# Performance work log

Measured on AMD Instinct MI355X. Metric: run time of the kernel, lower is better.

## Reference

```python
import jax, jax.numpy as jnp
import numpy as np

B, S, D = 1, 4096, 896
NH, NKV, HD = 14, 2, 64
ROPE_BASE = 1000000.0

def rotate_half(x):
    x1, x2 = x[..., :x.shape[-1] // 2], x[..., x.shape[-1] // 2:]
    return jnp.concatenate((-x2, x1), axis=-1)

def rope_tables(seq_len, head_dim, base):
    inv_freq = 1.0 / (base ** (jnp.arange(0, head_dim, 2, dtype=jnp.float32) / head_dim))
    t = jnp.arange(seq_len, dtype=jnp.float32)
    freqs = jnp.einsum('i,j->ij', t, inv_freq)
    emb = jnp.concatenate((freqs, freqs), axis=-1)  # [S, HD]
    return jnp.cos(emb), jnp.sin(emb)

def setup_inputs() -> dict:
    key = jax.random.key(0)
    ks = jax.random.split(key, 6)
    hidden_states = jax.random.normal(ks[0], (B, S, D), dtype=jnp.float32)
    # additive causal mask [1,1,S,S]
    neg = jnp.finfo(jnp.float32).min
    causal = jnp.where(jnp.tril(jnp.ones((S, S), dtype=bool)), 0.0, neg)
    attention_mask = causal[None, None, :, :].astype(jnp.float32)
    sc = 0.02
    Wq = jax.random.normal(ks[1], (D, NH * HD), dtype=jnp.float32) * sc
    Wk = jax.random.normal(ks[2], (D, NKV * HD), dtype=jnp.float32) * sc
    Wv = jax.random.normal(ks[3], (D, NKV * HD), dtype=jnp.float32) * sc
    Wo = jax.random.normal(ks[4], (D, D), dtype=jnp.float32) * sc
    bq = jnp.zeros((NH * HD,), jnp.float32)
    bk = jnp.zeros((NKV * HD,), jnp.float32)
    bv = jnp.zeros((NKV * HD,), jnp.float32)
    return {"hidden_states": hidden_states, "attention_mask": attention_mask,
            "Wq": Wq, "bq": bq, "Wk": Wk, "bk": bk, "Wv": Wv, "bv": bv, "Wo": Wo}

def reference(hidden_states, attention_mask, Wq, bq, Wk, bk, Wv, bv, Wo):
    b, s, _ = hidden_states.shape
    groups = NH // NKV
    q = (hidden_states @ Wq + bq).reshape(b, s, NH, HD)
    k = (hidden_states @ Wk + bk).reshape(b, s, NKV, HD)
    v = (hidden_states @ Wv + bv).reshape(b, s, NKV, HD)
    cos, sin = rope_tables(s, HD, ROPE_BASE)
    cos = cos[None, :, None, :]
    sin = sin[None, :, None, :]
    q = q * cos + rotate_half(q) * sin
    k = k * cos + rotate_half(k) * sin
    # GQA: repeat KV heads
    k = jnp.repeat(k, groups, axis=2)
    v = jnp.repeat(v, groups, axis=2)
    # [b, h, s, d]
    q = jnp.transpose(q, (0, 2, 1, 3))
    k = jnp.transpose(k, (0, 2, 1, 3))
    v = jnp.transpose(v, (0, 2, 1, 3))
    attn = jnp.einsum('bhqd,bhkd->bhqk', q, k) / jnp.sqrt(jnp.float32(HD))
    attn = attn + attention_mask
    attn = jax.nn.softmax(attn, axis=-1)
    out = jnp.einsum('bhqk,bhkd->bhqd', attn, v)
    out = jnp.transpose(out, (0, 2, 1, 3)).reshape(b, s, NH * HD)
    return out @ Wo
```

## Files before the change

### kernel.cpp

```cpp
#include <hip/hip_runtime.h>
#include <math.h>

constexpr int S_    = 4096;
constexpr int Dm    = 896;
constexpr int NHd   = 14;
constexpr int NKVh  = 2;
constexpr int HDim  = 64;
constexpr int NQ    = NHd * HDim;
constexpr int NK    = NKVh * HDim;
constexpr int NQK   = NQ + NK;
constexpr int GROUPS = NHd / NKVh;
constexpr float L2B   = 19.9315685693241740873f;
constexpr float LOG2E = 1.44269504088896340736f;

constexpr int NUNITS = 952;

typedef __attribute__((ext_vector_type(8)))  short bf16x8;
typedef __attribute__((ext_vector_type(4)))  short bf16x4;
typedef __attribute__((ext_vector_type(4)))  float f32x4;
typedef __attribute__((ext_vector_type(16))) float f32x16;
typedef __attribute__((ext_vector_type(4)))  int   i32x4;

__device__ __forceinline__ short f2bf(float f) {
  unsigned u = __builtin_bit_cast(unsigned, f);
  unsigned r = (u + 0x7FFFu + ((u >> 16) & 1u)) >> 16;
  return (short)r;
}
__device__ __forceinline__ float bf2f(short s) {
  return __builtin_bit_cast(float, ((unsigned)(unsigned short)s) << 16);
}

__device__ __forceinline__ unsigned cvtpk(float lo, float hi) {
  unsigned r;
  asm("v_cvt_pk_bf16_f32 %0, %1, %2" : "=v"(r) : "v"(lo), "v"(hi));
  return r;
}

__device__ __forceinline__ void gload16(const void* g, void* l) {
  __builtin_amdgcn_global_load_lds(
      (const __attribute__((address_space(1))) unsigned int*)g,
      (__attribute__((address_space(3))) unsigned int*)l, 16, 0, 0);
}

__global__ __launch_bounds__(256) void prep_all(
    const float* __restrict__ hs, short* __restrict__ hsb,
    float* __restrict__ cost, float* __restrict__ sint,
    const float* __restrict__ Wq, const float* __restrict__ Wk,
    const float* __restrict__ Wv, const float* __restrict__ Wo,
    short* __restrict__ wtq, short* __restrict__ wto,
    unsigned* __restrict__ cnt)
{
  const int bid = blockIdx.x;
  const int tid = threadIdx.x;
  if (bid == 2751 && tid == 0) *cnt = 0u;
  if (bid < 1792) {
    int idx = bid * 256 + tid;
    float4 a = ((const float4*)hs)[idx * 2];
    float4 b = ((const float4*)hs)[idx * 2 + 1];
    bf16x8 o;
    o[0] = f2bf(a.x); o[1] = f2bf(a.y); o[2] = f2bf(a.z); o[3] = f2bf(a.w);
    o[4] = f2bf(b.x); o[5] = f2bf(b.y); o[6] = f2bf(b.z); o[7] = f2bf(b.w);
    ((bf16x8*)hsb)[idx] = o;
    return;
  }
  if (bid < 2304) {
    int idx = (bid - 1792) * 256 + tid;
    int m = idx >> 5, j = idx & 31;
    float invf = exp2f(-(float)j * (L2B / 32.0f));
    float th = (float)m * invf;
    float s, c;
    sincosf(th, &s, &c);
    cost[idx] = c;
    sint[idx] = s;
    return;
  }
  __shared__ float t[64 * 68];
  const int b2 = bid - 2304;
  const int kt = b2 % 14;
  const int by = b2 / 14;

  const float* src; int srcN, nt; short* dst; int rowOff;
  if (by < 14)      { src = Wq; srcN = NQ; nt = by;      dst = wtq; rowOff = 0; }
  else if (by < 16) { src = Wk; srcN = NK; nt = by - 14; dst = wtq; rowOff = 896; }
  else if (by < 18) { src = Wv; srcN = NK; nt = by - 16; dst = wtq; rowOff = 1024; }
  else              { src = Wo; srcN = NQ; nt = by - 18; dst = wto; rowOff = 0; }

  #pragma unroll
  for (int i = 0; i < 4; i++) {
    int idx = tid + i * 256;
    int r = idx >> 4, c4 = (idx & 15) * 4;
    *(float4*)&t[r * 68 + c4] =
        *(const float4*)&src[(size_t)(kt * 64 + r) * srcN + nt * 64 + c4];
  }
  __syncthreads();
  const int nl = tid >> 2;
  const int kc = (tid & 3) * 16;
  bf16x8 o0, o1;
  #pragma unroll
  for (int i = 0; i < 8; i++) o0[i] = f2bf(t[(kc + i) * 68 + nl]);
  #pragma unroll
  for (int i = 0; i < 8; i++) o1[i] = f2bf(t[(kc + 8 + i) * 68 + nl]);
  short* dp = dst + (size_t)(rowOff + nt * 64 + nl) * 896 + kt * 64 + kc;
  *(bf16x8*)dp = o0;
  *(bf16x8*)(dp + 8) = o1;
}

template<int EPI>
__global__ __launch_bounds__(256) void gemm64(
    const short* __restrict__ A, const short* __restrict__ Bt,
    const float* __restrict__ biasq, const float* __restrict__ biask,
    const float* __restrict__ biasv,
    const float* __restrict__ cost, const float* __restrict__ sint,
    short* __restrict__ qkb, short* __restrict__ vtb,
    float* __restrict__ outp)
{
  __shared__ short Als[64 * 64];
  __shared__ short Bls[128 * 64];
  const int tid = threadIdx.x;
  const int lane = tid & 63;
  const int w = tid >> 6;
  const int wm = w >> 1, wn = w & 1;
  const int r16 = lane & 15, rg = lane >> 4;
  const int bm = blockIdx.x, bn = blockIdx.y;

  const f32x4 zero4 = {0.f, 0.f, 0.f, 0.f};
  f32x4 acc[2][4];
  #pragma unroll
  for (int mt = 0; mt < 2; mt++)
    #pragma unroll
    for (int nt = 0; nt < 4; nt++) acc[mt][nt] = zero4;

  const int srow = (lane >> 3);
  const int scol = (lane & 7) * 8;

  for (int kt = 0; kt < 14; ++kt) {
    __syncthreads();
    #pragma unroll
    for (int i = 0; i < 2; i++) {
      int c = w * 2 + i;
      int row = c * 8 + srow;
      gload16(A + (size_t)(bm * 64 + row) * 896 + kt * 64 + scol, &Als[c * 512]);
    }
    #pragma unroll
    for (int i = 0; i < 4; i++) {
      int c = w * 4 + i;
      int row = c * 8 + srow;
      gload16(Bt + (size_t)(bn * 128 + row) * 896 + kt * 64 + scol, &Bls[c * 512]);
    }
    __syncthreads();

    bf16x8 af[2][2], bfr[4][2];
    #pragma unroll
    for (int mt = 0; mt < 2; mt++)
      #pragma unroll
      for (int ks = 0; ks < 2; ks++)
        af[mt][ks] = *(const bf16x8*)&Als[(wm * 32 + mt * 16 + r16) * 64 + ks * 32 + rg * 8];
    #pragma unroll
    for (int nt = 0; nt < 4; nt++)
      #pragma unroll
      for (int ks = 0; ks < 2; ks++)
        bfr[nt][ks] = *(const bf16x8*)&Bls[(wn * 64 + nt * 16 + r16) * 64 + ks * 32 + rg * 8];
    #pragma unroll
    for (int mt = 0; mt < 2; mt++)
      #pragma unroll
      for (int nt = 0; nt < 4; nt++)
        #pragma unroll
        for (int ks = 0; ks < 2; ks++)
          acc[mt][nt] = __builtin_amdgcn_mfma_f32_16x16x32_bf16(
              af[mt][ks], bfr[nt][ks], acc[mt][nt], 0, 0, 0);
  }

  if (EPI == 0) {
    const int nbase = bn * 128 + wn * 64;
    if (bn < 8) {
      const float scl = (bn < 7) ? (0.125f * LOG2E) : 1.0f;
      const float* bias = (bn < 7) ? biasq : (biask - 896);
      #pragma unroll
      for (int mt = 0; mt < 2; mt++) {
        const int m0 = bm * 64 + wm * 32 + mt * 16 + rg * 4;
        #pragma unroll
        for (int nt = 0; nt < 4; nt++) {
          int n = nbase + nt * 16 + r16;
          int j = n & 31;
          float sgn = (n & 32) ? 1.f : -1.f;
          float b0 = bias[n], b1 = bias[n ^ 32];
          #pragma unroll
          for (int r = 0; r < 4; r++) {
            int m = m0 + r;
            float c_ = cost[m * 32 + j], s_ = sint[m * 32 + j];
            float val = ((acc[mt][nt][r] + b0) * c_ +
                         sgn * (acc[mt][nt ^ 2][r] + b1) * s_) * scl;
            qkb[(size_t)m * NQK + n] = f2bf(val);
          }
        }
      }
    } else {
      #pragma unroll
      for (int mt = 0; mt < 2; mt++) {
        const int m0 = bm * 64 + wm * 32 + mt * 16 + rg * 4;
        #pragma unroll
        for (int nt = 0; nt < 4; nt++) {
          int vc = wn * 64 + nt * 16 + r16;
          float b0 = biasv[vc];
          bf16x4 pk;
          #pragma unroll
          for (int r = 0; r < 4; r++) pk[r] = f2bf(acc[mt][nt][r] + b0);
          *(bf16x4*)&vtb[(size_t)vc * S_ + m0] = pk;
        }
      }
    }
  } else {
    #pragma unroll
    for (int mt = 0; mt < 2; mt++) {
      const int m0 = bm * 64 + wm * 32 + mt * 16 + rg * 4;
      #pragma unroll
      for (int nt = 0; nt < 4; nt++) {
        int n = bn * 128 + wn * 64 + nt * 16 + r16;
        #pragma unroll
        for (int r = 0; r < 4; r++)
          outp[(size_t)(m0 + r) * NQ + n] = acc[mt][nt][r];
      }
    }
  }
}

__global__ __launch_bounds__(256, 3) void flash_mfma(
    const short* __restrict__ qkb, const short* __restrict__ vtb,
    short* __restrict__ attnb, short* __restrict__ orec,
    float* __restrict__ mlrec, unsigned* __restrict__ cnt)
{
  __shared__ __align__(16) char lds[32768];
  __shared__ int s_unit;

  const int tid  = threadIdx.x;
  const int lane = tid & 63;
  const int w    = tid >> 6;
  const int q32  = lane & 31;
  const int hi   = lane >> 5;

  const int c8   = tid & 7;
  const int key0 = tid >> 3;
  const int key1 = key0 + 32;
  const int swz0 = (c8 ^ (key0 & 7)) << 4;
  const int swz1 = (c8 ^ (key1 & 7)) << 4;

  bf16x8 ones;
  #pragma unroll
  for (int j = 0; j < 8; j++) ones[j] = (short)0x3F80;

  for (;;) {
    __syncthreads();
    if (tid == 0) s_unit = (int)atomicAdd(cnt, 1u);
    __syncthreads();
    const int u = s_unit;
    if (u >= NUNITS) break;

    const int e = u / 14;
    const int h = u - e * 14;
    int qt, ci;
    if (e < 36)      { qt = 31 - e / 3; ci = e - (31 - qt) * 3; }
    else if (e < 60) { int f = e - 36; qt = 19 - (f >> 1); ci = f & 1; }
    else             { qt = 67 - e; ci = 0; }
    const int K  = 2 * (qt + 1);
    const int n  = (qt < 8) ? 1 : (qt < 20) ? 2 : 3;
    const int L  = (K + n - 1) / n;
    const int kt_lo = ci * L;
    const int kt_hi = (kt_lo + L < K) ? (kt_lo + L) : K;
    const int kv = h / GROUPS;
    const int q0 = qt * 128;
    const int kbase2 = (NQ + kv * HDim) * 2;
    const int qg = q0 + w * 32 + q32;

    bf16x8 qf[4];
    {
      const short* qp = qkb + (size_t)qg * NQK + h * HDim + hi * 8;
      #pragma unroll
      for (int ks = 0; ks < 4; ++ks) qf[ks] = *(const bf16x8*)(qp + ks * 16);
    }

    f32x16 acc_o[2], acc_l;
    float m_run = 0.f;
    #pragma unroll
    for (int r = 0; r < 16; ++r) { acc_o[0][r] = 0.f; acc_o[1][r] = 0.f; acc_l[r] = 0.f; }

    const char* ksrc0 = (const char*)qkb + (size_t)(kt_lo * 64 + key0) * 2048 + kbase2 + swz0;
    const char* ksrc1 = (const char*)qkb + (size_t)(kt_lo * 64 + key1) * 2048 + kbase2 + swz1;
    const char* vsrc0 = (const char*)vtb + (size_t)(kv * 64 + key0) * 8192 + (size_t)kt_lo * 128 + swz0;
    const char* vsrc1 = (const char*)vtb + (size_t)(kv * 64 + key1) * 8192 + (size_t)kt_lo * 128 + swz1;

    gload16(ksrc0, lds + w * 1024);
    gload16(ksrc1, lds + 4096 + w * 1024);
    gload16(vsrc0, lds + 8192 + w * 1024);
    gload16(vsrc1, lds + 12288 + w * 1024);
    ksrc0 += 131072; ksrc1 += 131072;
    vsrc0 += 128;    vsrc1 += 128;

    for (int kt = kt_lo; kt < kt_hi; ++kt) {
      const int cur = (kt - kt_lo) & 1;
      asm volatile("s_waitcnt vmcnt(0)" ::: "memory");
      __builtin_amdgcn_s_barrier();
      if (kt + 1 < kt_hi) {
        char* B = lds + ((cur ^ 1) << 14);
        gload16(ksrc0, B + w * 1024);
        gload16(ksrc1, B + 4096 + w * 1024);
        gload16(vsrc0, B + 8192 + w * 1024);
        gload16(vsrc1, B + 12288 + w * 1024);
        ksrc0 += 131072; ksrc1 += 131072;
        vsrc0 += 128;    vsrc1 += 128;
      }
      __builtin_amdgcn_sched_barrier(0);
      const char* KsB = lds + (cur << 14);
      const char* VtB = KsB + 8192;
      const int kb = kt * 64;

      f32x16 sc[2];
      #pragma unroll
      for (int r = 0; r < 16; ++r) { sc[0][r] = 0.f; sc[1][r] = 0.f; }
      #pragma unroll
      for (int t = 0; t < 2; ++t) {
        const int key = t * 32 + q32;
        #pragma unroll
        for (int ks = 0; ks < 4; ++ks) {
          bf16x8 kf = *(const bf16x8*)(KsB + key * 128 + (((2 * ks + hi) ^ (key & 7)) << 4));
          sc[t] = __builtin_amdgcn_mfma_f32_32x32x16_bf16(kf, qf[ks], sc[t], 0, 0, 0);
        }
      }

      if (kb + 63 > q0 + w * 32) {
        #pragma unroll
        for (int t = 0; t < 2; ++t)
          #pragma unroll
          for (int r = 0; r < 16; ++r) {
            int key = kb + t * 32 + (r & 3) + 8 * (r >> 2) + 4 * hi;
            sc[t][r] = (key > qg) ? -1e30f : sc[t][r];
          }
      }

      f32x16 mm;
      #pragma unroll
      for (int r = 0; r < 16; ++r) mm[r] = fmaxf(sc[0][r], sc[1][r]);
      #pragma unroll
      for (int r = 0; r < 8; ++r) mm[r] = fmaxf(mm[r], mm[r + 8]);
      #pragma unroll
      for (int r = 0; r < 4; ++r) mm[r] = fmaxf(mm[r], mm[r + 4]);
      float pm = fmaxf(fmaxf(mm[0], mm[1]), fmaxf(mm[2], mm[3]));
      {
        float a = pm, b = pm;
        asm("v_permlane32_swap_b32 %0, %1" : "+v"(a), "+v"(b));
        pm = fmaxf(a, b);
      }

      if (!__all(pm <= m_run + 8.0f)) {
        float newm = fmaxf(m_run, pm);
        float scl = exp2f(m_run - newm);
        m_run = newm;
        acc_l[0] *= scl;
        #pragma unroll
        for (int r = 0; r < 16; ++r) { acc_o[0][r] *= scl; acc_o[1][r] *= scl; }
      }

      #pragma unroll
      for (int t = 0; t < 2; ++t)
        #pragma unroll
        for (int r = 0; r < 16; ++r) sc[t][r] = exp2f(sc[t][r] - m_run);

      unsigned U0[2][4], U1[2][4];
      #pragma unroll
      for (int t = 0; t < 2; ++t)
        #pragma unroll
        for (int a = 0; a < 4; ++a) {
          U0[t][a] = cvtpk(sc[t][4 * a],     sc[t][4 * a + 1]);
          U1[t][a] = cvtpk(sc[t][4 * a + 2], sc[t][4 * a + 3]);
        }

      #pragma unroll
      for (int kp = 0; kp < 4; ++kp) {
        const int t = kp >> 1, c = kp & 1;
        unsigned x0 = U0[t][2 * c], y0 = U0[t][2 * c + 1];
        unsigned x1 = U1[t][2 * c], y1 = U1[t][2 * c + 1];
        asm("v_permlane32_swap_b32 %0, %1" : "+v"(x0), "+v"(y0));
        asm("v_permlane32_swap_b32 %0, %1" : "+v"(x1), "+v"(y1));
        i32x4 pi = {(int)x0, (int)x1, (int)y0, (int)y1};
        bf16x8 pf = __builtin_bit_cast(bf16x8, pi);
        acc_l = __builtin_amdgcn_mfma_f32_32x32x16_bf16(ones, pf, acc_l, 0, 0, 0);
        #pragma unroll
        for (int dt = 0; dt < 2; ++dt) {
          const int d = dt * 32 + q32;
          bf16x8 vf = *(const bf16x8*)(VtB + d * 128 + (((2 * kp + hi) ^ (d & 7)) << 4));
          acc_o[dt] = __builtin_amdgcn_mfma_f32_32x32x16_bf16(vf, pf, acc_o[dt], 0, 0, 0);
        }
      }
    }

    if (n == 1) {
      const float inv = 1.0f / acc_l[0];
      short* op = attnb + (size_t)qg * NQ + h * HDim + 4 * hi;
      #pragma unroll
      for (int dt = 0; dt < 2; ++dt)
        #pragma unroll
        for (int rq = 0; rq < 4; ++rq) {
          bf16x4 pk;
          pk[0] = f2bf(acc_o[dt][4 * rq]     * inv);
          pk[1] = f2bf(acc_o[dt][4 * rq + 1] * inv);
          pk[2] = f2bf(acc_o[dt][4 * rq + 2] * inv);
          pk[3] = f2bf(acc_o[dt][4 * rq + 3] * inv);
          *(bf16x4*)(op + dt * 32 + 8 * rq) = pk;
        }
    } else {
      const int qloc = w * 32 + q32;
      short* op;
      if (ci == 0) {
        op = attnb + (size_t)qg * NQ + h * HDim + 4 * hi;
      } else {
        int er = (qt < 20) ? (h * 36 + (qt - 8))
                           : (h * 36 + 12 + (qt - 20) * 2 + (ci - 1));
        op = orec + (size_t)er * 8192 + (size_t)qloc * 64 + 4 * hi;
      }
      #pragma unroll
      for (int dt = 0; dt < 2; ++dt)
        #pragma unroll
        for (int rq = 0; rq < 4; ++rq) {
          bf16x4 pk;
          pk[0] = f2bf(acc_o[dt][4 * rq]);
          pk[1] = f2bf(acc_o[dt][4 * rq + 1]);
          pk[2] = f2bf(acc_o[dt][4 * rq + 2]);
          pk[3] = f2bf(acc_o[dt][4 * rq + 3]);
          *(bf16x4*)(op + dt * 32 + 8 * rq) = pk;
        }
      if (hi == 0) {
        int co = (qt < 20) ? (8 + (qt - 8) * 2 + ci) : (32 + (qt - 20) * 3 + ci);
        float2 ml = {m_run, acc_l[0]};
        *(float2*)(mlrec + ((size_t)(h * 68 + co) * 128 + qloc) * 2) = ml;
      }
    }
  }
}

__global__ __launch_bounds__(128) void merge_chunks(
    const short* __restrict__ orec, const float* __restrict__ mlrec,
    short* __restrict__ attnb)
{
  const int b = blockIdx.x;
  const int h = b / 24;
  const int qt = 8 + (b - h * 24);
  const int n = (qt < 20) ? 2 : 3;
  const int qloc = threadIdx.x;
  const int q = qt * 128 + qloc;

  const int co0 = (qt < 20) ? (8 + (qt - 8) * 2) : (32 + (qt - 20) * 3);
  float2 ml0 = *(const float2*)(mlrec + ((size_t)(h * 68 + co0)     * 128 + qloc) * 2);
  float2 ml1 = *(const float2*)(mlrec + ((size_t)(h * 68 + co0 + 1) * 128 + qloc) * 2);
  float2 ml2 = (n == 3)
      ? *(const float2*)(mlrec + ((size_t)(h * 68 + co0 + 2) * 128 + qloc) * 2)
      : float2{-3.0e38f, 0.f};

  float M = fmaxf(fmaxf(ml0.x, ml1.x), ml2.x);
  float a0 = exp2f(ml0.x - M), a1 = exp2f(ml1.x - M);
  float a2 = (n == 3) ? exp2f(ml2.x - M) : 0.f;
  float inv = 1.0f / (a0 * ml0.y + a1 * ml1.y + a2 * ml2.y);
  float s0 = a0 * inv, s1 = a1 * inv, s2 = a2 * inv;

  const int er1 = (qt < 20) ? (h * 36 + (qt - 8)) : (h * 36 + 12 + (qt - 20) * 2);
  short* O0 = attnb + (size_t)q * NQ + h * HDim;
  const short* O1 = orec + (size_t)er1 * 8192 + (size_t)qloc * 64;
  const short* O2 = (n == 3) ? (O1 + 8192) : O1;

  #pragma unroll
  for (int i = 0; i < 8; i++) {
    bf16x8 x0 = *(const bf16x8*)(O0 + i * 8);
    bf16x8 x1 = *(const bf16x8*)(O1 + i * 8);
    bf16x8 x2 = *(const bf16x8*)(O2 + i * 8);
    bf16x8 o;
    #pragma unroll
    for (int j = 0; j < 8; j++)
      o[j] = f2bf(s0 * bf2f(x0[j]) + s1 * bf2f(x1[j]) + s2 * bf2f(x2[j]));
    *(bf16x8*)(O0 + i * 8) = o;
  }
}

extern "C" void kernel_launch(void* const* d_in, const int* in_sizes, int n_in,
                              void* d_out, int out_size, void* d_ws, size_t ws_size,
                              hipStream_t stream)
{
  const float* hs = (const float*)d_in[0];
  const float* Wq = (const float*)d_in[2];
  const float* bq = (const float*)d_in[3];
  const float* Wk = (const float*)d_in[4];
  const float* bk = (const float*)d_in[5];
  const float* Wv = (const float*)d_in[6];
  const float* bv = (const float*)d_in[7];
  const float* Wo = (const float*)d_in[8];

  short* hsb  = (short*)d_ws;
  short* wtq  = hsb + (size_t)S_ * Dm;
  short* wto  = wtq + (size_t)1152 * 896;
  float* cost = (float*)(wto + (size_t)896 * 896);
  float* sint = cost + (size_t)S_ * 32;
  short* qkb  = (short*)(sint + (size_t)S_ * 32);
  short* vtb  = qkb + (size_t)S_ * NQK;
  short* attnb= vtb + (size_t)NK * S_;
  float* out  = (float*)d_out;

  short*    orec  = hsb;
  float*    mlrec = cost;
  unsigned* cnt   = (unsigned*)((char*)attnb + (size_t)S_ * NQ * 2);

  hipLaunchKernelGGL(prep_all, dim3(2752), dim3(256), 0, stream,
                     hs, hsb, cost, sint, Wq, Wk, Wv, Wo, wtq, wto, cnt);
  hipLaunchKernelGGL((gemm64<0>), dim3(64, 9), dim3(256), 0, stream,
                     hsb, wtq, bq, bk, bv, cost, sint, qkb, vtb, (float*)nullptr);
  hipLaunchKernelGGL(flash_mfma, dim3(768), dim3(256), 0, stream,
                     qkb, vtb, attnb, orec, mlrec, cnt);
  hipLaunchKernelGGL(merge_chunks, dim3(336), dim3(128), 0, stream,
                     orec, mlrec, attnb);
  hipLaunchKernelGGL((gemm64<1>), dim3(64, 7), dim3(256), 0, stream,
                     attnb, wto, bq, bk, bv, cost, sint,
                     (short*)nullptr, (short*)nullptr, out);
}
```

Baseline: 130.0 us.

## Stage two KV tiles per barrier in flash attention and lower occupancy

The flash attention loop now loads and computes K/V tiles in pairs. A double buffer of two 64-key tiles per stage in a 64KB LDS array halves the number of vmcnt waits and block barriers. To make room for the larger LDS footprint, launch bounds drop from 3 to 2 blocks per SM and the persistent grid shrinks from 768 to 512 blocks. This trades latency hiding from occupancy for fewer synchronisation points and deeper prefetch; each barrier now waits on a larger batch of loads.

After: 131.6 us. No clear change (+1.2%).

```diff
diff --git a/kernel.cpp b/kernel.cpp
--- a/kernel.cpp
+++ b/kernel.cpp
@@ -224,12 +224,12 @@
   }
 }
 
-__global__ __launch_bounds__(256, 3) void flash_mfma(
+__global__ __launch_bounds__(256, 2) void flash_mfma(
     const short* __restrict__ qkb, const short* __restrict__ vtb,
     short* __restrict__ attnb, short* __restrict__ orec,
     float* __restrict__ mlrec, unsigned* __restrict__ cnt)
 {
-  __shared__ __align__(16) char lds[32768];
+  __shared__ __align__(16) char lds[65536];
   __shared__ int s_unit;
 
   const int tid  = threadIdx.x;
@@ -288,31 +288,16 @@
     const char* vsrc0 = (const char*)vtb + (size_t)(kv * 64 + key0) * 8192 + (size_t)kt_lo * 128 + swz0;
     const char* vsrc1 = (const char*)vtb + (size_t)(kv * 64 + key1) * 8192 + (size_t)kt_lo * 128 + swz1;
 
-    gload16(ksrc0, lds + w * 1024);
-    gload16(ksrc1, lds + 4096 + w * 1024);
-    gload16(vsrc0, lds + 8192 + w * 1024);
-    gload16(vsrc1, lds + 12288 + w * 1024);
-    ksrc0 += 131072; ksrc1 += 131072;
-    vsrc0 += 128;    vsrc1 += 128;
-
-    for (int kt = kt_lo; kt < kt_hi; ++kt) {
-      const int cur = (kt - kt_lo) & 1;
-      asm volatile("s_waitcnt vmcnt(0)" ::: "memory");
-      __builtin_amdgcn_s_barrier();
-      if (kt + 1 < kt_hi) {
-        char* B = lds + ((cur ^ 1) << 14);
-        gload16(ksrc0, B + w * 1024);
-        gload16(ksrc1, B + 4096 + w * 1024);
-        gload16(vsrc0, B + 8192 + w * 1024);
-        gload16(vsrc1, B + 12288 + w * 1024);
-        ksrc0 += 131072; ksrc1 += 131072;
-        vsrc0 += 128;    vsrc1 += 128;
-      }
-      __builtin_amdgcn_sched_barrier(0);
-      const char* KsB = lds + (cur << 14);
-      const char* VtB = KsB + 8192;
-      const int kb = kt * 64;
-
+    auto stage_tile = [&](char* base) {
+      gload16(ksrc0, base + w * 1024);
+      gload16(ksrc1, base + 4096 + w * 1024);
+      gload16(vsrc0, base + 8192 + w * 1024);
+      gload16(vsrc1, base + 12288 + w * 1024);
+      ksrc0 += 131072; ksrc1 += 131072;
+      vsrc0 += 128;    vsrc1 += 128;
+    };
+
+    auto compute_tile = [&](const char* KsB, const char* VtB, int kb) {
       f32x16 sc[2];
       #pragma unroll
       for (int r = 0; r < 16; ++r) { sc[0][r] = 0.f; sc[1][r] = 0.f; }
@@ -390,6 +375,26 @@
           acc_o[dt] = __builtin_amdgcn_mfma_f32_32x32x16_bf16(vf, pf, acc_o[dt], 0, 0, 0);
         }
       }
+    };
+
+    stage_tile(lds);
+    if (kt_lo + 1 < kt_hi) stage_tile(lds + 16384);
+
+    int cur = 0;
+    for (int kt = kt_lo; kt < kt_hi; kt += 2) {
+      asm volatile("s_waitcnt vmcnt(0)" ::: "memory");
+      __builtin_amdgcn_s_barrier();
+      if (kt + 2 < kt_hi) {
+        char* P = lds + ((cur ^ 1) << 15);
+        stage_tile(P);
+        if (kt + 3 < kt_hi) stage_tile(P + 16384);
+      }
+      __builtin_amdgcn_sched_barrier(0);
+      const char* base = lds + (cur << 15);
+      compute_tile(base, base + 8192, kt * 64);
+      if (kt + 1 < kt_hi)
+        compute_tile(base + 16384, base + 24576, (kt + 1) * 64);
+      cur ^= 1;
     }
 
     if (n == 1) {
@@ -509,7 +514,7 @@
                      hs, hsb, cost, sint, Wq, Wk, Wv, Wo, wtq, wto, cnt);
   hipLaunchKernelGGL((gemm64<0>), dim3(64, 9), dim3(256), 0, stream,
                      hsb, wtq, bq, bk, bv, cost, sint, qkb, vtb, (float*)nullptr);
-  hipLaunchKernelGGL(flash_mfma, dim3(768), dim3(256), 0, stream,
+  hipLaunchKernelGGL(flash_mfma, dim3(512), dim3(256), 0, stream,
                      qkb, vtb, attnb, orec, mlrec, cnt);
   hipLaunchKernelGGL(merge_chunks, dim3(336), dim3(128), 0, stream,
                      orec, mlrec, attnb);
```
